# Kernel optimization log

Hardware: AMD Instinct MI355X
Metric: run time of the kernel (lower is better)

Reference implementation:

```python
import jax, jax.numpy as jnp
import numpy as np


def setup_inputs() -> dict:
    key = jax.random.key(0)
    k1, k2, k3, k4, k5 = jax.random.split(key, 5)
    B, Te, Td, De, Dd = 8, 256, 256, 512, 512
    return {
        "encoder_out_seq": jax.random.normal(k1, (B, Te, De), dtype=jnp.float32),
        "decoder_out_seq": jax.random.normal(k2, (B, Td, Dd), dtype=jnp.float32),
        "W_a": jax.random.normal(k3, (De, De), dtype=jnp.float32) * 0.05,
        "U_a": jax.random.normal(k4, (Dd, De), dtype=jnp.float32) * 0.05,
        "V_a": jax.random.normal(k5, (De, 1), dtype=jnp.float32) * 0.05,
    }


def reference(encoder_out_seq, decoder_out_seq, W_a, U_a, V_a):
    # Bahdanau additive attention, fully vectorized over decoder timesteps
    # (replaces the two sequential K.rnn scans in the original).
    Ws = jnp.einsum('bte,ef->btf', encoder_out_seq, W_a)   # [B,Te,De]
    Uh = jnp.einsum('bqd,df->bqf', decoder_out_seq, U_a)   # [B,Td,De]
    # scores[b,q,t] = tanh(Ws[b,t,:] + Uh[b,q,:]) . V_a
    scores = jnp.einsum('bqtf,f->bqt',
                        jnp.tanh(Ws[:, None, :, :] + Uh[:, :, None, :]),
                        V_a[:, 0])                          # [B,Td,Te]
    e = jax.nn.softmax(scores, axis=-1)                     # attention weights
    c = jnp.einsum('bqt,btf->bqf', e, encoder_out_seq)      # context vectors
    return (c, e)
```

## Files before the change

### kernel.cpp

```cpp
#include <hip/hip_runtime.h>

#define NB 8
#define TE 256
#define TD 256
#define DE 512
#define QT 4

#define K2SCALE 2.8853900817779268f

typedef short bf16x8 __attribute__((ext_vector_type(8)));
typedef float f32x4 __attribute__((ext_vector_type(4)));
typedef unsigned short u16x8 __attribute__((ext_vector_type(8)));

static __device__ __forceinline__ unsigned short f2bf(float x) {
  unsigned int u = __float_as_uint(x);
  u += 0x7fffu + ((u >> 16) & 1u);
  return (unsigned short)(u >> 16);
}

static __device__ __forceinline__ void split8(
    const float4& x0, const float4& x1, u16x8& h, u16x8& l) {
  float xs[8] = {x0.x, x0.y, x0.z, x0.w, x1.x, x1.y, x1.z, x1.w};
  #pragma unroll
  for (int j = 0; j < 8; ++j) {
    unsigned int u = __float_as_uint(xs[j]);
    h[j] = (unsigned short)(u >> 16);
    float hf = __uint_as_float(u & 0xffff0000u);
    l[j] = f2bf(xs[j] - hf);
  }
}

__global__ __launch_bounds__(256) void convB(
    const float* __restrict__ w0, unsigned short* __restrict__ h0, unsigned short* __restrict__ l0,
    const float* __restrict__ w1, unsigned short* __restrict__ h1, unsigned short* __restrict__ l1)
{
  const float* W = blockIdx.z ? w1 : w0;
  unsigned short* H = blockIdx.z ? h1 : h0;
  unsigned short* L = blockIdx.z ? l1 : l0;
  __shared__ unsigned short sh[32][33], sl[32][33];
  const int t = threadIdx.x;
  const int k0 = blockIdx.y * 32, n0 = blockIdx.x * 32;
  const int r = t >> 3, c = (t & 7) * 4;
  float4 x = *(const float4*)(W + (size_t)(k0 + r) * DE + n0 + c);
  float xs[4] = {x.x, x.y, x.z, x.w};
  #pragma unroll
  for (int j = 0; j < 4; ++j) {
    unsigned short hh = f2bf(xs[j]);
    float hf = __uint_as_float((unsigned int)hh << 16);
    sh[r][c + j] = hh;
    sl[r][c + j] = f2bf(xs[j] - hf);
  }
  __syncthreads();
  ushort4 oh, ol;
  oh.x = sh[c + 0][r]; oh.y = sh[c + 1][r]; oh.z = sh[c + 2][r]; oh.w = sh[c + 3][r];
  ol.x = sl[c + 0][r]; ol.y = sl[c + 1][r]; ol.z = sl[c + 2][r]; ol.w = sl[c + 3][r];
  *(ushort4*)(H + (size_t)(n0 + r) * DE + k0 + c) = oh;
  *(ushort4*)(L + (size_t)(n0 + r) * DE + k0 + c) = ol;
}

__global__ __launch_bounds__(256) void gemm_mfma(
    const float* __restrict__ A0,
    const unsigned short* __restrict__ BH0, const unsigned short* __restrict__ BL0,
    float* __restrict__ C0,
    const float* __restrict__ A1,
    const unsigned short* __restrict__ BH1, const unsigned short* __restrict__ BL1,
    float* __restrict__ C1)
{
  const float*          A  = blockIdx.z ? A1  : A0;
  const unsigned short* BH = blockIdx.z ? BH1 : BH0;
  const unsigned short* BL = blockIdx.z ? BL1 : BL0;
  float*                C  = blockIdx.z ? C1  : C0;
  const int tid  = threadIdx.x;
  const int lane = tid & 63;
  const int wave = tid >> 6;
  const int wm = wave >> 1, wn = wave & 1;
  const int g = lane >> 4, r16 = lane & 15;
  const int m0 = blockIdx.y * 128, n0 = blockIdx.x * 64;
  __shared__ __align__(16) unsigned short Ah[2][128][40], Al[2][128][40];
  __shared__ __align__(16) unsigned short Bh[2][64][40],  Bl[2][64][40];
  const int arow = tid >> 2;
  const int apart = (tid & 3) * 8;

  float4 a00, a01, a10, a11;
  u16x8 pb, plb;
#define LOADTILE(KT) do {                                                   \
    const size_t ko = (size_t)(KT) * 32 + apart;                            \
    const float* pa_ = A + (size_t)(m0 + arow) * 512 + ko;                  \
    a00 = *(const float4*)pa_;       a01 = *(const float4*)(pa_ + 4);       \
    a10 = *(const float4*)(pa_ + 64 * 512);                                 \
    a11 = *(const float4*)(pa_ + 64 * 512 + 4);                             \
    pb  = *(const u16x8*)(BH + (size_t)(n0 + arow) * 512 + ko);             \
    plb = *(const u16x8*)(BL + (size_t)(n0 + arow) * 512 + ko);             \
  } while (0)
#define STORETILE(BUF) do {                                                 \
    u16x8 h0_, l0_, h1_, l1_;                                               \
    split8(a00, a01, h0_, l0_);                                             \
    split8(a10, a11, h1_, l1_);                                             \
    *(u16x8*)&Ah[BUF][arow][apart] = h0_;                                   \
    *(u16x8*)&Ah[BUF][arow + 64][apart] = h1_;                              \
    *(u16x8*)&Al[BUF][arow][apart] = l0_;                                   \
    *(u16x8*)&Al[BUF][arow + 64][apart] = l1_;                              \
    *(u16x8*)&Bh[BUF][arow][apart] = pb;                                    \
    *(u16x8*)&Bl[BUF][arow][apart] = plb;                                   \
  } while (0)

  f32x4 accm[4][2], acce[4][2];
  #pragma unroll
  for (int mt = 0; mt < 4; ++mt)
    #pragma unroll
    for (int nt = 0; nt < 2; ++nt) {
      accm[mt][nt] = (f32x4){0.f, 0.f, 0.f, 0.f};
      acce[mt][nt] = (f32x4){0.f, 0.f, 0.f, 0.f};
    }

  LOADTILE(0);
  STORETILE(0);
  __syncthreads();

  for (int kt = 0; kt < 16; ++kt) {
    const int cur = kt & 1;
    if (kt + 1 < 16) LOADTILE(kt + 1);
    bf16x8 ah[4], al[4], bh[2], bl[2];
    #pragma unroll
    for (int mt = 0; mt < 4; ++mt) {
      ah[mt] = *(const bf16x8*)&Ah[cur][wm * 64 + mt * 16 + r16][g * 8];
      al[mt] = *(const bf16x8*)&Al[cur][wm * 64 + mt * 16 + r16][g * 8];
    }
    #pragma unroll
    for (int nt = 0; nt < 2; ++nt) {
      bh[nt] = *(const bf16x8*)&Bh[cur][wn * 32 + nt * 16 + r16][g * 8];
      bl[nt] = *(const bf16x8*)&Bl[cur][wn * 32 + nt * 16 + r16][g * 8];
    }
    #pragma unroll
    for (int mt = 0; mt < 4; ++mt)
      #pragma unroll
      for (int nt = 0; nt < 2; ++nt) {
        accm[mt][nt] = __builtin_amdgcn_mfma_f32_16x16x32_bf16(ah[mt], bh[nt], accm[mt][nt], 0, 0, 0);
        acce[mt][nt] = __builtin_amdgcn_mfma_f32_16x16x32_bf16(al[mt], bh[nt], acce[mt][nt], 0, 0, 0);
        acce[mt][nt] = __builtin_amdgcn_mfma_f32_16x16x32_bf16(ah[mt], bl[nt], acce[mt][nt], 0, 0, 0);
      }
    if (kt + 1 < 16) STORETILE(cur ^ 1);
    __syncthreads();
  }
#undef LOADTILE
#undef STORETILE

  #pragma unroll
  for (int mt = 0; mt < 4; ++mt)
    #pragma unroll
    for (int nt = 0; nt < 2; ++nt)
      #pragma unroll
      for (int j = 0; j < 4; ++j) {
        float vsum = accm[mt][nt][j] + acce[mt][nt][j];
        int row = m0 + wm * 64 + mt * 16 + g * 4 + j;
        int col = n0 + wn * 32 + nt * 16 + r16;
        C[(size_t)row * 512 + col] = __builtin_amdgcn_exp2f(vsum * K2SCALE);
      }
}

__global__ __launch_bounds__(512) void attn(
    const float* __restrict__ ws, const float* __restrict__ uh,
    const float* __restrict__ enc, const float* __restrict__ va,
    float* __restrict__ out_c, float* __restrict__ out_e)
{
  const int tid  = threadIdx.x;
  const int wave = tid >> 6;
  const int lane = tid & 63;
  const int b  = blockIdx.x >> 6;
  const int q0 = (blockIdx.x & 63) * QT;
  __shared__ float s_sc[QT][TE];
  __shared__ float red[3][QT][DE];
  const int fbase = lane * 8;

  float4 v0 = *(const float4*)(va + fbase);
  float4 v1 = *(const float4*)(va + fbase + 4);
  float v[8] = {v0.x, v0.y, v0.z, v0.w, v1.x, v1.y, v1.z, v1.w};

  float eu[QT][8];
  #pragma unroll
  for (int q = 0; q < QT; ++q) {
    const float* up = uh + (size_t)(b * TD + q0 + q) * DE + fbase;
    float4 u0 = *(const float4*)(up);
    float4 u1 = *(const float4*)(up + 4);
    eu[q][0] = u0.x; eu[q][1] = u0.y; eu[q][2] = u0.z; eu[q][3] = u0.w;
    eu[q][4] = u1.x; eu[q][5] = u1.y; eu[q][6] = u1.z; eu[q][7] = u1.w;
  }

  const int t0 = wave * 32;
  const float* wp = ws + (size_t)(b * TE + t0) * DE + fbase;
  float4 w0 = *(const float4*)(wp);
  float4 w1 = *(const float4*)(wp + 4);
  for (int t = t0; t < t0 + 32; ++t) {
    float cw[8] = {w0.x, w0.y, w0.z, w0.w, w1.x, w1.y, w1.z, w1.w};
    wp += DE;
    w0 = *(const float4*)(wp);
    w1 = *(const float4*)(wp + 4);
    float a[QT];
    #pragma unroll
    for (int q = 0; q < QT; ++q) {
      float A0 = fmaf(cw[0], eu[q][0], 1.f);
      float A1 = fmaf(cw[1], eu[q][1], 1.f);
      float A2 = fmaf(cw[2], eu[q][2], 1.f);
      float A3 = fmaf(cw[3], eu[q][3], 1.f);
      float B0 = fmaf(cw[4], eu[q][4], 1.f);
      float B1 = fmaf(cw[5], eu[q][5], 1.f);
      float B2 = fmaf(cw[6], eu[q][6], 1.f);
      float B3 = fmaf(cw[7], eu[q][7], 1.f);
      float n1 = fmaf(v[1], A0, v[0] * A1);
      float d1 = A0 * A1;
      float n2 = fmaf(v[3], A2, v[2] * A3);
      float d2 = A2 * A3;
      float N1 = fmaf(n2, d1, n1 * d2);
      float D1 = d1 * d2;
      float n3 = fmaf(v[5], B0, v[4] * B1);
      float d3 = B0 * B1;
      float n4 = fmaf(v[7], B2, v[6] * B3);
      float d4 = B2 * B3;
      float N2 = fmaf(n4, d3, n3 * d4);
      float D2 = d3 * d4;
      float s = N1 * __builtin_amdgcn_rcpf(D1);
      a[q] = fmaf(N2, __builtin_amdgcn_rcpf(D2), s);
    }
    {
      const bool h1 = lane & 1;
      float m0 = h1 ? a[1] : a[0], o0 = h1 ? a[0] : a[1];
      float m1 = h1 ? a[3] : a[2], o1 = h1 ? a[2] : a[3];
      float r0 = m0 + __shfl_xor(o0, 1, 64);
      float r1 = m1 + __shfl_xor(o1, 1, 64);
      const bool h2 = lane & 2;
      float mm = h2 ? r1 : r0, oo = h2 ? r0 : r1;
      float r = mm + __shfl_xor(oo, 2, 64);
      r += __shfl_xor(r, 4, 64);
      r += __shfl_xor(r, 8, 64);
      r += __shfl_xor(r, 16, 64);
      r += __shfl_xor(r, 32, 64);
      if (lane < QT) s_sc[lane][t] = -2.f * r;
    }
  }
  __syncthreads();

  if (wave < QT) {
    const int r = wave;
    float x[4];
    #pragma unroll
    for (int i = 0; i < 4; ++i) x[i] = s_sc[r][lane + 64 * i];
    float m = fmaxf(fmaxf(x[0], x[1]), fmaxf(x[2], x[3]));
    #pragma unroll
    for (int off = 32; off >= 1; off >>= 1) m = fmaxf(m, __shfl_xor(m, off, 64));
    const float L2E = 1.4426950408889634f;
    float ssum = 0.f;
    #pragma unroll
    for (int i = 0; i < 4; ++i) { x[i] = __builtin_amdgcn_exp2f((x[i] - m) * L2E); ssum += x[i]; }
    #pragma unroll
    for (int off = 32; off >= 1; off >>= 1) ssum += __shfl_xor(ssum, off, 64);
    float inv = 1.f / ssum;
    float* oe = out_e + (size_t)(b * TD + q0 + r) * TE;
    #pragma unroll
    for (int i = 0; i < 4; ++i) {
      float e = x[i] * inv;
      s_sc[r][lane + 64 * i] = e;
      oe[lane + 64 * i] = e;
    }
  }
  __syncthreads();

  {
    const int fgrp = tid >> 7;
    const int f4   = (tid & 127) * 4;
    float4 c[QT];
    #pragma unroll
    for (int q = 0; q < QT; ++q) c[q] = make_float4(0.f, 0.f, 0.f, 0.f);
    const float* eb = enc + (size_t)b * TE * DE + f4;
    const int tb = fgrp * 64;
    #pragma unroll 4
    for (int t = tb; t < tb + 64; ++t) {
      float4 ee = *(const float4*)(eb + (size_t)t * DE);
      #pragma unroll
      for (int q = 0; q < QT; ++q) {
        float w = s_sc[q][t];
        c[q].x = fmaf(w, ee.x, c[q].x);
        c[q].y = fmaf(w, ee.y, c[q].y);
        c[q].z = fmaf(w, ee.z, c[q].z);
        c[q].w = fmaf(w, ee.w, c[q].w);
      }
    }
    if (fgrp > 0) {
      #pragma unroll
      for (int q = 0; q < QT; ++q) *(float4*)&red[fgrp - 1][q][f4] = c[q];
    }
    __syncthreads();
    if (fgrp == 0) {
      #pragma unroll
      for (int q = 0; q < QT; ++q) {
        float4 r1 = *(const float4*)&red[0][q][f4];
        float4 r2 = *(const float4*)&red[1][q][f4];
        float4 r3 = *(const float4*)&red[2][q][f4];
        c[q].x += (r1.x + r2.x) + r3.x;
        c[q].y += (r1.y + r2.y) + r3.y;
        c[q].z += (r1.z + r2.z) + r3.z;
        c[q].w += (r1.w + r2.w) + r3.w;
        *(float4*)(out_c + (size_t)(b * TD + q0 + q) * DE + f4) = c[q];
      }
    }
  }
}

extern "C" void kernel_launch(void* const* d_in, const int* in_sizes, int n_in,
                              void* d_out, int out_size, void* d_ws, size_t ws_size,
                              hipStream_t stream) {
  const float* enc = (const float*)d_in[0];
  const float* dec = (const float*)d_in[1];
  const float* Wa  = (const float*)d_in[2];
  const float* Ua  = (const float*)d_in[3];
  const float* Va  = (const float*)d_in[4];
  float* out_c = (float*)d_out;
  float* out_e = out_c + (size_t)NB * TD * DE;

  float* ws = (float*)d_ws;
  float* uh = ws + 1048576;
  unsigned short* BHw = (unsigned short*)(uh + 1048576);
  unsigned short* BLw = BHw + 262144;
  unsigned short* BHu = BLw + 262144;
  unsigned short* BLu = BHu + 262144;

  convB<<<dim3(16, 16, 2), dim3(256), 0, stream>>>(Wa, BHw, BLw, Ua, BHu, BLu);
  gemm_mfma<<<dim3(8, 16, 2), dim3(256), 0, stream>>>(
      enc, BHw, BLw, ws, dec, BHu, BLu, uh);
  attn<<<dim3(NB * (TD / QT)), dim3(512), 0, stream>>>(
      ws, uh, enc, Va, out_c, out_e);
}
```

Before: 72.09 us.

## Shrink GEMM M-tile, batch score reduction across four timesteps, round hi split

```diff
diff --git a/kernel.cpp b/kernel.cpp
--- a/kernel.cpp
+++ b/kernel.cpp
@@ -23,9 +23,9 @@
   float xs[8] = {x0.x, x0.y, x0.z, x0.w, x1.x, x1.y, x1.z, x1.w};
   #pragma unroll
   for (int j = 0; j < 8; ++j) {
-    unsigned int u = __float_as_uint(xs[j]);
-    h[j] = (unsigned short)(u >> 16);
-    float hf = __uint_as_float(u & 0xffff0000u);
+    unsigned short hh = f2bf(xs[j]);
+    float hf = __uint_as_float((unsigned int)hh << 16);
+    h[j] = hh;
     l[j] = f2bf(xs[j] - hf);
   }
 }
@@ -75,38 +75,33 @@
   const int wave = tid >> 6;
   const int wm = wave >> 1, wn = wave & 1;
   const int g = lane >> 4, r16 = lane & 15;
-  const int m0 = blockIdx.y * 128, n0 = blockIdx.x * 64;
-  __shared__ __align__(16) unsigned short Ah[2][128][40], Al[2][128][40];
-  __shared__ __align__(16) unsigned short Bh[2][64][40],  Bl[2][64][40];
+  const int m0 = blockIdx.y * 64, n0 = blockIdx.x * 64;
+  __shared__ __align__(16) unsigned short Ah[2][64][40], Al[2][64][40];
+  __shared__ __align__(16) unsigned short Bh[2][64][40], Bl[2][64][40];
   const int arow = tid >> 2;
   const int apart = (tid & 3) * 8;
 
-  float4 a00, a01, a10, a11;
+  float4 a00, a01;
   u16x8 pb, plb;
 #define LOADTILE(KT) do {                                                   \
     const size_t ko = (size_t)(KT) * 32 + apart;                            \
     const float* pa_ = A + (size_t)(m0 + arow) * 512 + ko;                  \
-    a00 = *(const float4*)pa_;       a01 = *(const float4*)(pa_ + 4);       \
-    a10 = *(const float4*)(pa_ + 64 * 512);                                 \
-    a11 = *(const float4*)(pa_ + 64 * 512 + 4);                             \
+    a00 = *(const float4*)pa_;  a01 = *(const float4*)(pa_ + 4);            \
     pb  = *(const u16x8*)(BH + (size_t)(n0 + arow) * 512 + ko);             \
     plb = *(const u16x8*)(BL + (size_t)(n0 + arow) * 512 + ko);             \
   } while (0)
 #define STORETILE(BUF) do {                                                 \
-    u16x8 h0_, l0_, h1_, l1_;                                               \
+    u16x8 h0_, l0_;                                                         \
     split8(a00, a01, h0_, l0_);                                             \
-    split8(a10, a11, h1_, l1_);                                             \
     *(u16x8*)&Ah[BUF][arow][apart] = h0_;                                   \
-    *(u16x8*)&Ah[BUF][arow + 64][apart] = h1_;                              \
     *(u16x8*)&Al[BUF][arow][apart] = l0_;                                   \
-    *(u16x8*)&Al[BUF][arow + 64][apart] = l1_;                              \
     *(u16x8*)&Bh[BUF][arow][apart] = pb;                                    \
     *(u16x8*)&Bl[BUF][arow][apart] = plb;                                   \
   } while (0)
 
-  f32x4 accm[4][2], acce[4][2];
-  #pragma unroll
-  for (int mt = 0; mt < 4; ++mt)
+  f32x4 accm[2][2], acce[2][2];
+  #pragma unroll
+  for (int mt = 0; mt < 2; ++mt)
     #pragma unroll
     for (int nt = 0; nt < 2; ++nt) {
       accm[mt][nt] = (f32x4){0.f, 0.f, 0.f, 0.f};
@@ -120,11 +115,11 @@
   for (int kt = 0; kt < 16; ++kt) {
     const int cur = kt & 1;
     if (kt + 1 < 16) LOADTILE(kt + 1);
-    bf16x8 ah[4], al[4], bh[2], bl[2];
-    #pragma unroll
-    for (int mt = 0; mt < 4; ++mt) {
-      ah[mt] = *(const bf16x8*)&Ah[cur][wm * 64 + mt * 16 + r16][g * 8];
-      al[mt] = *(const bf16x8*)&Al[cur][wm * 64 + mt * 16 + r16][g * 8];
+    bf16x8 ah[2], al[2], bh[2], bl[2];
+    #pragma unroll
+    for (int mt = 0; mt < 2; ++mt) {
+      ah[mt] = *(const bf16x8*)&Ah[cur][wm * 32 + mt * 16 + r16][g * 8];
+      al[mt] = *(const bf16x8*)&Al[cur][wm * 32 + mt * 16 + r16][g * 8];
     }
     #pragma unroll
     for (int nt = 0; nt < 2; ++nt) {
@@ -132,7 +127,7 @@
       bl[nt] = *(const bf16x8*)&Bl[cur][wn * 32 + nt * 16 + r16][g * 8];
     }
     #pragma unroll
-    for (int mt = 0; mt < 4; ++mt)
+    for (int mt = 0; mt < 2; ++mt)
       #pragma unroll
       for (int nt = 0; nt < 2; ++nt) {
         accm[mt][nt] = __builtin_amdgcn_mfma_f32_16x16x32_bf16(ah[mt], bh[nt], accm[mt][nt], 0, 0, 0);
@@ -146,19 +141,19 @@
 #undef STORETILE
 
   #pragma unroll
-  for (int mt = 0; mt < 4; ++mt)
+  for (int mt = 0; mt < 2; ++mt)
     #pragma unroll
     for (int nt = 0; nt < 2; ++nt)
       #pragma unroll
       for (int j = 0; j < 4; ++j) {
         float vsum = accm[mt][nt][j] + acce[mt][nt][j];
-        int row = m0 + wm * 64 + mt * 16 + g * 4 + j;
+        int row = m0 + wm * 32 + mt * 16 + g * 4 + j;
         int col = n0 + wn * 32 + nt * 16 + r16;
         C[(size_t)row * 512 + col] = __builtin_amdgcn_exp2f(vsum * K2SCALE);
       }
 }
 
-__global__ __launch_bounds__(512) void attn(
+__global__ __launch_bounds__(512, 4) void attn(
     const float* __restrict__ ws, const float* __restrict__ uh,
     const float* __restrict__ enc, const float* __restrict__ va,
     float* __restrict__ out_c, float* __restrict__ out_e)
@@ -187,55 +182,72 @@
   }
 
   const int t0 = wave * 32;
-  const float* wp = ws + (size_t)(b * TE + t0) * DE + fbase;
-  float4 w0 = *(const float4*)(wp);
-  float4 w1 = *(const float4*)(wp + 4);
-  for (int t = t0; t < t0 + 32; ++t) {
-    float cw[8] = {w0.x, w0.y, w0.z, w0.w, w1.x, w1.y, w1.z, w1.w};
-    wp += DE;
-    w0 = *(const float4*)(wp);
-    w1 = *(const float4*)(wp + 4);
-    float a[QT];
-    #pragma unroll
-    for (int q = 0; q < QT; ++q) {
-      float A0 = fmaf(cw[0], eu[q][0], 1.f);
-      float A1 = fmaf(cw[1], eu[q][1], 1.f);
-      float A2 = fmaf(cw[2], eu[q][2], 1.f);
-      float A3 = fmaf(cw[3], eu[q][3], 1.f);
-      float B0 = fmaf(cw[4], eu[q][4], 1.f);
-      float B1 = fmaf(cw[5], eu[q][5], 1.f);
-      float B2 = fmaf(cw[6], eu[q][6], 1.f);
-      float B3 = fmaf(cw[7], eu[q][7], 1.f);
-      float n1 = fmaf(v[1], A0, v[0] * A1);
-      float d1 = A0 * A1;
-      float n2 = fmaf(v[3], A2, v[2] * A3);
-      float d2 = A2 * A3;
-      float N1 = fmaf(n2, d1, n1 * d2);
-      float D1 = d1 * d2;
-      float n3 = fmaf(v[5], B0, v[4] * B1);
-      float d3 = B0 * B1;
-      float n4 = fmaf(v[7], B2, v[6] * B3);
-      float d4 = B2 * B3;
-      float N2 = fmaf(n4, d3, n3 * d4);
-      float D2 = d3 * d4;
-      float s = N1 * __builtin_amdgcn_rcpf(D1);
-      a[q] = fmaf(N2, __builtin_amdgcn_rcpf(D2), s);
-    }
-    {
-      const bool h1 = lane & 1;
-      float m0 = h1 ? a[1] : a[0], o0 = h1 ? a[0] : a[1];
-      float m1 = h1 ? a[3] : a[2], o1 = h1 ? a[2] : a[3];
-      float r0 = m0 + __shfl_xor(o0, 1, 64);
-      float r1 = m1 + __shfl_xor(o1, 1, 64);
-      const bool h2 = lane & 2;
-      float mm = h2 ? r1 : r0, oo = h2 ? r0 : r1;
-      float r = mm + __shfl_xor(oo, 2, 64);
-      r += __shfl_xor(r, 4, 64);
-      r += __shfl_xor(r, 8, 64);
-      r += __shfl_xor(r, 16, 64);
-      r += __shfl_xor(r, 32, 64);
-      if (lane < QT) s_sc[lane][t] = -2.f * r;
-    }
+  const float* wsb = ws + (size_t)b * TE * DE + fbase;
+  for (int tt = t0; tt < t0 + 32; tt += 4) {
+    float wr[4][8];
+    #pragma unroll
+    for (int dt = 0; dt < 4; ++dt) {
+      const float* wp = wsb + (size_t)(tt + dt) * DE;
+      float4 w0 = *(const float4*)(wp);
+      float4 w1 = *(const float4*)(wp + 4);
+      wr[dt][0] = w0.x; wr[dt][1] = w0.y; wr[dt][2] = w0.z; wr[dt][3] = w0.w;
+      wr[dt][4] = w1.x; wr[dt][5] = w1.y; wr[dt][6] = w1.z; wr[dt][7] = w1.w;
+    }
+    float a[16];
+    #pragma unroll
+    for (int dt = 0; dt < 4; ++dt)
+      #pragma unroll
+      for (int q = 0; q < QT; ++q) {
+        float A0 = fmaf(wr[dt][0], eu[q][0], 1.f);
+        float A1 = fmaf(wr[dt][1], eu[q][1], 1.f);
+        float A2 = fmaf(wr[dt][2], eu[q][2], 1.f);
+        float A3 = fmaf(wr[dt][3], eu[q][3], 1.f);
+        float B0 = fmaf(wr[dt][4], eu[q][4], 1.f);
+        float B1 = fmaf(wr[dt][5], eu[q][5], 1.f);
+        float B2 = fmaf(wr[dt][6], eu[q][6], 1.f);
+        float B3 = fmaf(wr[dt][7], eu[q][7], 1.f);
+        float n1 = fmaf(v[1], A0, v[0] * A1);
+        float d1 = A0 * A1;
+        float n2 = fmaf(v[3], A2, v[2] * A3);
+        float d2 = A2 * A3;
+        float N1 = fmaf(n2, d1, n1 * d2);
+        float D1 = d1 * d2;
+        float n3 = fmaf(v[5], B0, v[4] * B1);
+        float d3 = B0 * B1;
+        float n4 = fmaf(v[7], B2, v[6] * B3);
+        float d4 = B2 * B3;
+        float N2 = fmaf(n4, d3, n3 * d4);
+        float D2 = d3 * d4;
+        float s = N1 * __builtin_amdgcn_rcpf(D1);
+        a[q + 4 * dt] = fmaf(N2, __builtin_amdgcn_rcpf(D2), s);
+      }
+    float b8[8];
+    #pragma unroll
+    for (int k = 0; k < 8; ++k) {
+      float mine = (lane & 1) ? a[2 * k + 1] : a[2 * k];
+      float oth  = (lane & 1) ? a[2 * k]     : a[2 * k + 1];
+      b8[k] = mine + __shfl_xor(oth, 1, 64);
+    }
+    float c4[4];
+    #pragma unroll
+    for (int k = 0; k < 4; ++k) {
+      float mine = (lane & 2) ? b8[2 * k + 1] : b8[2 * k];
+      float oth  = (lane & 2) ? b8[2 * k]     : b8[2 * k + 1];
+      c4[k] = mine + __shfl_xor(oth, 2, 64);
+    }
+    float d2v[2];
+    #pragma unroll
+    for (int k = 0; k < 2; ++k) {
+      float mine = (lane & 4) ? c4[2 * k + 1] : c4[2 * k];
+      float oth  = (lane & 4) ? c4[2 * k]     : c4[2 * k + 1];
+      d2v[k] = mine + __shfl_xor(oth, 4, 64);
+    }
+    float mine = (lane & 8) ? d2v[1] : d2v[0];
+    float oth  = (lane & 8) ? d2v[0] : d2v[1];
+    float e = mine + __shfl_xor(oth, 8, 64);
+    e += __shfl_xor(e, 16, 64);
+    e += __shfl_xor(e, 32, 64);
+    if (lane < 16) s_sc[lane & 3][tt + (lane >> 2)] = -2.f * e;
   }
   __syncthreads();
 
@@ -324,7 +336,7 @@
   unsigned short* BLu = BHu + 262144;
 
   convB<<<dim3(16, 16, 2), dim3(256), 0, stream>>>(Wa, BHw, BLw, Ua, BHu, BLu);
-  gemm_mfma<<<dim3(8, 16, 2), dim3(256), 0, stream>>>(
+  gemm_mfma<<<dim3(8, 32, 2), dim3(256), 0, stream>>>(
       enc, BHw, BLw, ws, dec, BHu, BLu, uh);
   attn<<<dim3(NB * (TD / QT)), dim3(512), 0, stream>>>(
       ws, uh, enc, Va, out_c, out_e);
```

Measured after the change: 69.01 us. -4.3%, faster.
